# Kernel optimization log

Hardware: AMD Instinct MI355X
Metric: run time of the kernel (lower is better)

Reference implementation:

```python
import jax, jax.numpy as jnp
import numpy as np

N_NODES = 100000
N_EDGES = 1600000
D_IN, D_H1, D_H2 = 128, 64, 16


def setup_inputs() -> dict:
    key = jax.random.key(0)
    ks = jax.random.split(key, 12)
    def glorot(k, shape):
        fan_in, fan_out = shape
        lim = np.sqrt(6.0 / (fan_in + fan_out)).astype(np.float32)
        return jax.random.uniform(k, shape, jnp.float32, -lim, lim)
    x = jax.random.normal(ks[0], (N_NODES, D_IN), jnp.float32)
    edge_index = jax.random.randint(ks[1], (2, N_EDGES), 0, N_NODES, jnp.int64)
    return {
        "x": x,
        "edge_index": edge_index,
        # SAGEConv1: lin_l (neighbor agg, has bias), lin_r (root, no bias) -- stored (in,out)
        "w1_l": glorot(ks[2], (D_IN, D_H1)),
        "w1_r": glorot(ks[3], (D_IN, D_H1)),
        "b1": jnp.zeros((D_H1,), jnp.float32),
        # SAGEConv2
        "w2_l": glorot(ks[4], (D_H1, D_H2)),
        "w2_r": glorot(ks[5], (D_H1, D_H2)),
        "b2": jnp.zeros((D_H2,), jnp.float32),
        # MLP head
        "fc1_w": glorot(ks[6], (D_H2, 8)),
        "fc1_b": jnp.zeros((8,), jnp.float32),
        "fc2_w": glorot(ks[7], (8, 1)),
        "fc2_b": jnp.zeros((1,), jnp.float32),
    }


def _sage_conv(h, src, dst, n_nodes, w_l, w_r, b):
    # mean aggregation of source-node features into destination nodes
    msgs = h[src]                                                  # [E, d]
    agg = jax.ops.segment_sum(msgs, dst, num_segments=n_nodes)     # [N, d]
    deg = jax.ops.segment_sum(jnp.ones((src.shape[0],), h.dtype), dst,
                              num_segments=n_nodes)                # [N]
    mean = agg / jnp.maximum(deg, 1.0)[:, None]
    return mean @ w_l + h @ w_r + b


def reference(x, edge_index, w1_l, w1_r, b1, w2_l, w2_r, b2,
              fc1_w, fc1_b, fc2_w, fc2_b):
    src, dst = edge_index[0], edge_index[1]
    n = x.shape[0]
    h = _sage_conv(x, src, dst, n, w1_l, w1_r, b1)   # [N, 64]
    h = _sage_conv(h, src, dst, n, w2_l, w2_r, b2)   # [N, 16]
    # embedding_mlp on edge endpoint embeddings
    e = h[src] * h[dst]                              # [E, 16]
    out = (e @ fc1_w + fc1_b) @ fc2_w + fc2_b        # [E, 1]
    return jax.nn.sigmoid(out)
```

## Files before the change

kernel.cpp:

```cpp
#include <hip/hip_runtime.h>
#include <hip/hip_fp16.h>
#include <math.h>

#define NN 100000
#define NE 1600000

#define BSH  9
#define BKN  512
#define NB   196
#define ABLK 128
#define EPB  ((NE + ABLK - 1) / ABLK)
#define GEMMB ((NN + 63) / 64)
#define GBLK ((GEMMB + 1) / 2)

typedef __attribute__((ext_vector_type(8))) short bf16x8;
typedef __attribute__((ext_vector_type(4))) float f32x4;

__device__ __forceinline__ unsigned short f2bf(float f) {
    unsigned u = __builtin_bit_cast(unsigned, f);
    u += 0x7fffu + ((u >> 16) & 1u);
    return (unsigned short)(u >> 16);
}
__device__ __forceinline__ float bf2f(unsigned short h) {
    unsigned u = ((unsigned)h) << 16;
    return __builtin_bit_cast(float, u);
}
__device__ __forceinline__ float2 unpackh2(unsigned w) {
    const __half2 h = __builtin_bit_cast(__half2, w);
    return __half22float2(h);
}

__global__ __launch_bounds__(256) void fused0(const int* __restrict__ dst,
    const float* __restrict__ w1l, const float* __restrict__ w1r,
    const float* __restrict__ w2l, const float* __restrict__ w2r,
    const float* __restrict__ b1, const float* __restrict__ fc1w,
    const float* __restrict__ fc1b, const float* __restrict__ fc2w,
    const float* __restrict__ fc2b, int* __restrict__ mat,
    unsigned short* __restrict__ ATh, unsigned short* __restrict__ ATl,
    float* __restrict__ cbuf)
{
    __shared__ int h[NB];
    __shared__ float sl[64], sr[64];
    const int t = threadIdx.x;
    if (blockIdx.x < ABLK) {
        for (int i = t; i < NB; i += 256) h[i] = 0;
        __syncthreads();
        const int a = blockIdx.x;
        const int beg = a * EPB;
        const int end = (beg + EPB < NE) ? beg + EPB : NE;
        for (int e = beg + t; e < end; e += 256)
            atomicAdd(&h[dst[e] >> BSH], 1);
        __syncthreads();
        for (int i = t; i < NB; i += 256) mat[(size_t)i * ABLK + a] = h[i];
        return;
    }
    if (blockIdx.x < ABLK + 128) {
        const int k = blockIdx.x - ABLK;
        const int j = t;
        if (j < 64) { sl[j] = w1l[k * 64 + j]; sr[j] = w1r[k * 64 + j]; }
        __syncthreads();
        if (j < 64) {
            const int sel = j >> 4, jj = j & 15;
            const float* row = (sel < 2) ? sl : sr;
            const float* w2  = (sel & 1) ? w2r : w2l;
            float acc = 0.f;
#pragma unroll
            for (int m = 0; m < 64; ++m) acc = fmaf(row[m], w2[m * 16 + jj], acc);
            const unsigned short hh = f2bf(acc);
            ATh[j * 128 + k] = hh;
            ATl[j * 128 + k] = f2bf(acc - bf2f(hh));
        }
        return;
    }
    const int j = t;
    if (j < 16) {
        float a = 0.f;
        for (int m = 0; m < 64; ++m) a = fmaf(b1[m], w2l[m * 16 + j], a);
        cbuf[j] = a;
    } else if (j < 32) {
        const int jj = j - 16;
        float a = 0.f;
        for (int m = 0; m < 64; ++m) a = fmaf(b1[m], w2r[m * 16 + jj], a);
        cbuf[j] = a;
    } else if (j < 48) {
        const int k = j - 32;
        float a = 0.f;
        for (int m = 0; m < 8; ++m) a = fmaf(fc1w[k * 8 + m], fc2w[m], a);
        cbuf[j] = a;
    } else if (j == 48) {
        float a = fc2b[0];
        for (int m = 0; m < 8; ++m) a = fmaf(fc1b[m], fc2w[m], a);
        cbuf[48] = a;
    }
}

__global__ __launch_bounds__(256) void scan_all(int* __restrict__ mat,
    int* __restrict__ bbase)
{
    __shared__ int s[256];
    const int t = threadIdx.x;
    int run = 0;
    if (t < NB) {
        int* col = mat + (size_t)t * ABLK;
        for (int a = 0; a < ABLK; ++a) { const int v = col[a]; col[a] = run; run += v; }
    }
    s[t] = (t < NB) ? run : 0;
    __syncthreads();
    for (int off = 1; off < 256; off <<= 1) {
        const int u = (t >= off) ? s[t - off] : 0;
        __syncthreads();
        s[t] += u;
        __syncthreads();
    }
    if (t < NB) bbase[t] = s[t] - run;
    if (t == NB - 1) bbase[NB] = s[t];
}

#define LDST 136
__global__ __launch_bounds__(512) void fused1(const int* __restrict__ src,
    const int* __restrict__ dst, const int* __restrict__ mat,
    const int* __restrict__ bbase, unsigned* __restrict__ part,
    const float* __restrict__ x, const unsigned short* __restrict__ ATh,
    const unsigned short* __restrict__ ATl, signed char* __restrict__ p8,
    float* __restrict__ pscale, __half* __restrict__ qh)
{
    __shared__ unsigned short sAh[64 * LDST];
    __shared__ unsigned short sAl[64 * LDST];
    __shared__ int cur[NB];
    const int tid = threadIdx.x;

    if (blockIdx.x < ABLK) {
        const int a = blockIdx.x;
        for (int i = tid; i < NB; i += 512)
            cur[i] = mat[(size_t)i * ABLK + a] + bbase[i];
        __syncthreads();
        const int beg = a * EPB;
        const int end = (beg + EPB < NE) ? beg + EPB : NE;
        for (int e = beg + tid; e < end; e += 512) {
            const int s = src[e], d = dst[e];
            const int pos = atomicAdd(&cur[d >> BSH], 1);
            part[pos] = ((unsigned)s << BSH) | (unsigned)(d & (BKN - 1));
        }
        return;
    }

    for (int i = tid; i < 1024; i += 512) {
        const int row = i >> 4, ch = i & 15;
        const uint4 vh = *(const uint4*)(ATh + row * 128 + ch * 8);
        const uint4 vl = *(const uint4*)(ATl + row * 128 + ch * 8);
        *(uint4*)(sAh + row * LDST + ch * 8) = vh;
        *(uint4*)(sAl + row * LDST + ch * 8) = vl;
    }
    __syncthreads();

    const int wave8 = tid >> 6;
    const int tile = (blockIdx.x - ABLK) * 2 + (wave8 >> 2);
    const int wave = wave8 & 3;
    const int lane = tid & 63;
    const int lr = lane & 15;
    const int lg = lane >> 4;

    bf16x8 bh[4][4], bl[4][4];
#pragma unroll
    for (int ct = 0; ct < 4; ++ct) {
        const int col = ct * 16 + lr;
#pragma unroll
        for (int ks = 0; ks < 4; ++ks) {
            const int k0 = ks * 32 + lg * 8;
            bh[ct][ks] = *(const bf16x8*)(sAh + col * LDST + k0);
            bl[ct][ks] = *(const bf16x8*)(sAl + col * LDST + k0);
        }
    }

    if (tile >= GEMMB) return;
    const int tilebase = tile * 64;
    const int xrowidx = tilebase + wave * 16 + lr;
    const float* xrow = x + (size_t)(xrowidx < NN ? xrowidx : NN - 1) * 128;

    f32x4 acc[4] = {f32x4{0,0,0,0}, f32x4{0,0,0,0}, f32x4{0,0,0,0}, f32x4{0,0,0,0}};
#pragma unroll
    for (int ks = 0; ks < 4; ++ks) {
        const int k0 = ks * 32 + lg * 8;
        const float4 v0 = *(const float4*)(xrow + k0);
        const float4 v1 = *(const float4*)(xrow + k0 + 4);
        const float vv[8] = {v0.x, v0.y, v0.z, v0.w, v1.x, v1.y, v1.z, v1.w};
        bf16x8 xh, xl;
#pragma unroll
        for (int j = 0; j < 8; ++j) {
            const unsigned short h = f2bf(vv[j]);
            xh[j] = (short)h;
            xl[j] = (short)f2bf(vv[j] - bf2f(h));
        }
#pragma unroll
        for (int ct = 0; ct < 4; ++ct) {
            acc[ct] = __builtin_amdgcn_mfma_f32_16x16x32_bf16(xh, bh[ct][ks], acc[ct], 0, 0, 0);
            acc[ct] = __builtin_amdgcn_mfma_f32_16x16x32_bf16(xh, bl[ct][ks], acc[ct], 0, 0, 0);
            acc[ct] = __builtin_amdgcn_mfma_f32_16x16x32_bf16(xl, bh[ct][ks], acc[ct], 0, 0, 0);
        }
    }

#pragma unroll
    for (int rg = 0; rg < 4; ++rg) {
        float m = fmaxf(fabsf(acc[0][rg]), fabsf(acc[1][rg]));
#pragma unroll
        for (int d = 1; d < 16; d <<= 1) m = fmaxf(m, __shfl_xor(m, d, 64));
        m = fmaxf(m, 1e-20f);
        const float scl = m * (1.0f / 127.0f);
        const float inv = 127.0f / m;
        const int nrow = tilebase + wave * 16 + lg * 4 + rg;
        if (nrow < NN) {
            const int q0 = __float2int_rn(acc[0][rg] * inv);
            const int q1 = __float2int_rn(acc[1][rg] * inv);
            p8[(size_t)nrow * 32 + lr]      = (signed char)q0;
            p8[(size_t)nrow * 32 + 16 + lr] = (signed char)q1;
            if (lr == 0) pscale[nrow] = scl;
            qh[(size_t)nrow * 32 + lr]      = __float2half(acc[2][rg]);
            qh[(size_t)nrow * 32 + 16 + lr] = __float2half(acc[3][rg]);
        }
    }
}

__global__ __launch_bounds__(512) void partB_build(const unsigned* __restrict__ part,
    const int* __restrict__ bbase, int* __restrict__ rowptr, int* __restrict__ cols)
{
    __shared__ int h[BKN];
    __shared__ int cur[BKN];
    __shared__ int wsum[8];
    const int b = blockIdx.x;
    const int t = threadIdx.x;
    const int beg = bbase[b], end = bbase[b + 1];
    h[t] = 0;
    __syncthreads();
    for (int e = beg + t; e < end; e += 512)
        atomicAdd(&h[part[e] & (BKN - 1u)], 1);
    __syncthreads();
    const int v = h[t];
    int inc = v;
#pragma unroll
    for (int d = 1; d < 64; d <<= 1) {
        const int u = __shfl_up(inc, d, 64);
        if ((t & 63) >= d) inc += u;
    }
    if ((t & 63) == 63) wsum[t >> 6] = inc;
    __syncthreads();
    int woff = 0;
    for (int w = 0; w < (t >> 6); ++w) woff += wsum[w];
    const int excl = inc + woff - v;
    cur[t] = excl;
    const int node = b * BKN + t;
    if (node < NN) rowptr[node] = beg + excl;
    if (b == NB - 1 && t == 0) rowptr[NN] = NE;
    __syncthreads();
    for (int e = beg + t; e < end; e += 512) {
        const unsigned w = part[e];
        const int pos = atomicAdd(&cur[w & (BKN - 1u)], 1);
        cols[beg + pos] = (int)(w >> BSH);
    }
}

__global__ __launch_bounds__(256) void agg1_csr(const int* __restrict__ rowptr,
    const int* __restrict__ cols, const signed char* __restrict__ p8,
    const float* __restrict__ pscale, const __half* __restrict__ qh,
    const float* __restrict__ cbuf, __half* __restrict__ g, __half* __restrict__ r)
{
    const int node = blockIdx.x * 8 + (threadIdx.x >> 5);
    if (node >= NN) return;
    const int lane = threadIdx.x & 31;
    const int es = lane >> 2;
    const int k  = lane & 3;
    const int beg = rowptr[node], end = rowptr[node + 1];
    const uint2* p64 = (const uint2*)p8;
    float a0 = 0.f, a1 = 0.f, a2 = 0.f, a3 = 0.f;
    float a4 = 0.f, a5 = 0.f, a6 = 0.f, a7 = 0.f;
#pragma unroll 2
    for (int j = beg; j < end; j += 8) {
        const int jj = j + es;
        const int s = cols[(jj < end) ? jj : (end - 1)];
        const float scl = (jj < end) ? pscale[s] : 0.f;
        const uint2 w = p64[(size_t)s * 4 + k];
        a0 = fmaf((float)(signed char)(w.x & 0xffu), scl, a0);
        a1 = fmaf((float)(signed char)((w.x >> 8) & 0xffu), scl, a1);
        a2 = fmaf((float)(signed char)((w.x >> 16) & 0xffu), scl, a2);
        a3 = fmaf((float)(signed char)(w.x >> 24), scl, a3);
        a4 = fmaf((float)(signed char)(w.y & 0xffu), scl, a4);
        a5 = fmaf((float)(signed char)((w.y >> 8) & 0xffu), scl, a5);
        a6 = fmaf((float)(signed char)((w.y >> 16) & 0xffu), scl, a6);
        a7 = fmaf((float)(signed char)(w.y >> 24), scl, a7);
    }
#pragma unroll
    for (int d = 4; d <= 16; d <<= 1) {
        a0 += __shfl_xor(a0, d, 64); a1 += __shfl_xor(a1, d, 64);
        a2 += __shfl_xor(a2, d, 64); a3 += __shfl_xor(a3, d, 64);
        a4 += __shfl_xor(a4, d, 64); a5 += __shfl_xor(a5, d, 64);
        a6 += __shfl_xor(a6, d, 64); a7 += __shfl_xor(a7, d, 64);
    }
    if (es == 0) {
        const float dg = (float)(end - beg);
        const float inv = 1.0f / fmaxf(dg, 1.0f);
        const uint4 qw = *(const uint4*)(qh + (size_t)node * 32 + 8 * k);
        const float2 q0 = unpackh2(qw.x), q1 = unpackh2(qw.y);
        const float2 q2 = unpackh2(qw.z), q3 = unpackh2(qw.w);
        const float4 cb0 = *(const float4*)(cbuf + 8 * k);
        const float4 cb1 = *(const float4*)(cbuf + 8 * k + 4);
        const float v0 = fmaf(a0, inv, q0.x + cb0.x);
        const float v1 = fmaf(a1, inv, q0.y + cb0.y);
        const float v2 = fmaf(a2, inv, q1.x + cb0.z);
        const float v3 = fmaf(a3, inv, q1.y + cb0.w);
        const float v4 = fmaf(a4, inv, q2.x + cb1.x);
        const float v5 = fmaf(a5, inv, q2.y + cb1.y);
        const float v6 = fmaf(a6, inv, q3.x + cb1.z);
        const float v7 = fmaf(a7, inv, q3.y + cb1.w);
        uint4 ow;
        ow.x = __builtin_bit_cast(unsigned, __floats2half2_rn(v0, v1));
        ow.y = __builtin_bit_cast(unsigned, __floats2half2_rn(v2, v3));
        ow.z = __builtin_bit_cast(unsigned, __floats2half2_rn(v4, v5));
        ow.w = __builtin_bit_cast(unsigned, __floats2half2_rn(v6, v7));
        if (k < 2) *(uint4*)(g + (size_t)node * 16 + 8 * k) = ow;
        else       *(uint4*)(r + (size_t)node * 16 + 8 * (k - 2)) = ow;
    }
}

__global__ __launch_bounds__(256) void agg2_csr(const int* __restrict__ rowptr,
    const int* __restrict__ cols, const __half* __restrict__ g,
    const __half* __restrict__ r, const float* __restrict__ b2,
    __half* __restrict__ h2)
{
    const int node = blockIdx.x * 8 + (threadIdx.x >> 5);
    if (node >= NN) return;
    const int lane = threadIdx.x & 31;
    const int es = lane >> 2;
    const int k  = lane & 3;
    const int beg = rowptr[node], end = rowptr[node + 1];
    const uint2* g64 = (const uint2*)g;
    float a0 = 0.f, a1 = 0.f, a2 = 0.f, a3 = 0.f;
#pragma unroll 2
    for (int j = beg; j < end; j += 8) {
        const int jj = j + es;
        const int s = cols[(jj < end) ? jj : (end - 1)];
        const float m = (jj < end) ? 1.0f : 0.0f;
        const uint2 w = g64[(size_t)s * 4 + k];
        const float2 v0 = unpackh2(w.x);
        const float2 v1 = unpackh2(w.y);
        a0 = fmaf(v0.x, m, a0);
        a1 = fmaf(v0.y, m, a1);
        a2 = fmaf(v1.x, m, a2);
        a3 = fmaf(v1.y, m, a3);
    }
#pragma unroll
    for (int d = 4; d <= 16; d <<= 1) {
        a0 += __shfl_xor(a0, d, 64); a1 += __shfl_xor(a1, d, 64);
        a2 += __shfl_xor(a2, d, 64); a3 += __shfl_xor(a3, d, 64);
    }
    if (es == 0) {
        const float dg = (float)(end - beg);
        const float inv = 1.0f / fmaxf(dg, 1.0f);
        const uint2 rw = ((const uint2*)r)[(size_t)node * 4 + k];
        const float2 r0 = unpackh2(rw.x), r1 = unpackh2(rw.y);
        const float4 bb = *(const float4*)(b2 + 4 * k);
        const float v0 = fmaf(a0, inv, r0.x + bb.x);
        const float v1 = fmaf(a1, inv, r0.y + bb.y);
        const float v2 = fmaf(a2, inv, r1.x + bb.z);
        const float v3 = fmaf(a3, inv, r1.y + bb.w);
        uint2 ow;
        ow.x = __builtin_bit_cast(unsigned, __floats2half2_rn(v0, v1));
        ow.y = __builtin_bit_cast(unsigned, __floats2half2_rn(v2, v3));
        ((uint2*)h2)[(size_t)node * 4 + k] = ow;
    }
}

__global__ __launch_bounds__(256) void edge_mlp(const int* __restrict__ src,
    const int* __restrict__ dst, const __half* __restrict__ h2,
    const float* __restrict__ cbuf, float* __restrict__ out)
{
    __shared__ float sv[17];
    if (threadIdx.x < 16) sv[threadIdx.x] = cbuf[32 + threadIdx.x];
    if (threadIdx.x == 16) sv[16] = cbuf[48];
    __syncthreads();
    const int e0 = blockIdx.x * 512 + threadIdx.x;
    const int e1 = e0 + 256;
    const int s0 = src[e0], d0 = dst[e0];
    const int s1 = src[e1], d1 = dst[e1];
    const uint4* hs0 = (const uint4*)(h2 + (size_t)s0 * 16);
    const uint4* hd0 = (const uint4*)(h2 + (size_t)d0 * 16);
    const uint4* hs1 = (const uint4*)(h2 + (size_t)s1 * 16);
    const uint4* hd1 = (const uint4*)(h2 + (size_t)d1 * 16);
    const uint4 a00 = hs0[0], a01 = hs0[1];
    const uint4 b00 = hd0[0], b01 = hd0[1];
    const uint4 a10 = hs1[0], a11 = hs1[1];
    const uint4 b10 = hd1[0], b11 = hd1[1];
    const unsigned aw0[8] = {a00.x, a00.y, a00.z, a00.w, a01.x, a01.y, a01.z, a01.w};
    const unsigned bw0[8] = {b00.x, b00.y, b00.z, b00.w, b01.x, b01.y, b01.z, b01.w};
    const unsigned aw1[8] = {a10.x, a10.y, a10.z, a10.w, a11.x, a11.y, a11.z, a11.w};
    const unsigned bw1[8] = {b10.x, b10.y, b10.z, b10.w, b11.x, b11.y, b11.z, b11.w};
    float acc0 = sv[16], acc1 = sv[16];
#pragma unroll
    for (int qq = 0; qq < 8; ++qq) {
        const float2 a0 = unpackh2(aw0[qq]), b0 = unpackh2(bw0[qq]);
        const float2 a1 = unpackh2(aw1[qq]), b1 = unpackh2(bw1[qq]);
        acc0 = fmaf(a0.x * b0.x, sv[qq * 2 + 0], acc0);
        acc0 = fmaf(a0.y * b0.y, sv[qq * 2 + 1], acc0);
        acc1 = fmaf(a1.x * b1.x, sv[qq * 2 + 0], acc1);
        acc1 = fmaf(a1.y * b1.y, sv[qq * 2 + 1], acc1);
    }
    out[e0] = 1.0f / (1.0f + __expf(-acc0));
    out[e1] = 1.0f / (1.0f + __expf(-acc1));
}

extern "C" void kernel_launch(void* const* d_in, const int* in_sizes, int n_in,
                              void* d_out, int out_size, void* d_ws, size_t ws_size,
                              hipStream_t stream)
{
    const float* x    = (const float*)d_in[0];
    const int*   ei   = (const int*)d_in[1];
    const float* w1l  = (const float*)d_in[2];
    const float* w1r  = (const float*)d_in[3];
    const float* b1   = (const float*)d_in[4];
    const float* w2l  = (const float*)d_in[5];
    const float* w2r  = (const float*)d_in[6];
    const float* b2   = (const float*)d_in[7];
    const float* fc1w = (const float*)d_in[8];
    const float* fc1b = (const float*)d_in[9];
    const float* fc2w = (const float*)d_in[10];
    const float* fc2b = (const float*)d_in[11];
    float* out = (float*)d_out;

    const int* src = ei;
    const int* dst = ei + NE;

    int* W = (int*)d_ws;
    size_t o = 0;
#define ALIGN16() o = (o + 15) & ~(size_t)15
    int* mat    = W + o; o += (size_t)NB * ABLK; ALIGN16();
    int* bbase  = W + o; o += NB + 1;            ALIGN16();
    int* rowptr = W + o; o += NN + 1;            ALIGN16();
    unsigned* part = (unsigned*)(W + o); o += NE; ALIGN16();
    int* cols   = W + o; o += NE;                ALIGN16();
    unsigned short* ATh = (unsigned short*)(W + o); o += 4096; ALIGN16();
    unsigned short* ATl = (unsigned short*)(W + o); o += 4096; ALIGN16();
    float* cbuf = (float*)(W + o); o += 64;      ALIGN16();
    signed char* p8 = (signed char*)(W + o); o += (size_t)NN * 8;  ALIGN16();
    float* pscale   = (float*)(W + o); o += NN;  ALIGN16();
    __half* qh  = (__half*)(W + o); o += (size_t)NN * 16; ALIGN16();
    __half* g   = (__half*)(W + o); o += (size_t)NN * 8;  ALIGN16();
    __half* r   = (__half*)(W + o); o += (size_t)NN * 8;  ALIGN16();
    __half* h2  = (__half*)(W + o); o += (size_t)NN * 8;  ALIGN16();

    fused0<<<ABLK + 129, 256, 0, stream>>>(dst, w1l, w1r, w2l, w2r, b1,
                                           fc1w, fc1b, fc2w, fc2b, mat, ATh, ATl, cbuf);
    scan_all<<<1, 256, 0, stream>>>(mat, bbase);
    fused1<<<ABLK + GBLK, 512, 0, stream>>>(src, dst, mat, bbase, part,
                                            x, ATh, ATl, p8, pscale, qh);
    partB_build<<<NB, 512, 0, stream>>>(part, bbase, rowptr, cols);
    agg1_csr<<<(NN + 7) / 8, 256, 0, stream>>>(rowptr, cols, p8, pscale, qh, cbuf, g, r);
    agg2_csr<<<(NN + 7) / 8, 256, 0, stream>>>(rowptr, cols, g, r, b2, h2);
    edge_mlp<<<NE / 512, 256, 0, stream>>>(src, dst, h2, cbuf, out);
}
```

Baseline: 141.7 us.

## Overlap CSR bucket build with layer-1 GEMM and widen CSR gather loads

The edge scatter becomes its own kernel. The per-bucket CSR build (histogram, scan, column placement) is merged into the projection GEMM kernel through a shared-memory union, so the CSR build can overlap with the dense GEMM instead of running as a separate serialized launch. Both aggregation kernels now gather 16-byte rows per lane instead of 8-byte rows, processing 16 edges per iteration and doing one more shuffle-reduction step. This trades more registers per lane and a longer reduction for fewer, wider memory transactions.

```diff
diff --git a/kernel.cpp b/kernel.cpp
--- a/kernel.cpp
+++ b/kernel.cpp
@@ -12,6 +12,7 @@
 #define EPB  ((NE + ABLK - 1) / ABLK)
 #define GEMMB ((NN + 63) / 64)
 #define GBLK ((GEMMB + 1) / 2)
+#define LDST 136
 
 typedef __attribute__((ext_vector_type(8))) short bf16x8;
 typedef __attribute__((ext_vector_type(4))) float f32x4;
@@ -29,6 +30,10 @@
     const __half2 h = __builtin_bit_cast(__half2, w);
     return __half22float2(h);
 }
+
+struct GemmSmem { unsigned short sAh[64 * LDST]; unsigned short sAl[64 * LDST]; };
+struct PartSmem { int h[BKN]; int cur[BKN]; int wsum[8]; };
+union FusedSmem { GemmSmem gm; PartSmem pb; };
 
 __global__ __launch_bounds__(256) void fused0(const int* __restrict__ dst,
     const float* __restrict__ w1l, const float* __restrict__ w1r,
@@ -116,34 +121,72 @@
     if (t == NB - 1) bbase[NB] = s[t];
 }
 
-#define LDST 136
-__global__ __launch_bounds__(512) void fused1(const int* __restrict__ src,
+__global__ __launch_bounds__(512) void partA_scatter(const int* __restrict__ src,
     const int* __restrict__ dst, const int* __restrict__ mat,
-    const int* __restrict__ bbase, unsigned* __restrict__ part,
+    const int* __restrict__ bbase, unsigned* __restrict__ part)
+{
+    __shared__ int cur[NB];
+    const int a = blockIdx.x;
+    for (int i = threadIdx.x; i < NB; i += 512)
+        cur[i] = mat[(size_t)i * ABLK + a] + bbase[i];
+    __syncthreads();
+    const int beg = a * EPB;
+    const int end = (beg + EPB < NE) ? beg + EPB : NE;
+    for (int e = beg + threadIdx.x; e < end; e += 512) {
+        const int s = src[e], d = dst[e];
+        const int pos = atomicAdd(&cur[d >> BSH], 1);
+        part[pos] = ((unsigned)s << BSH) | (unsigned)(d & (BKN - 1));
+    }
+}
+
+__global__ __launch_bounds__(512) void fused2(const unsigned* __restrict__ part,
+    const int* __restrict__ bbase, int* __restrict__ rowptr, int* __restrict__ cols,
     const float* __restrict__ x, const unsigned short* __restrict__ ATh,
     const unsigned short* __restrict__ ATl, signed char* __restrict__ p8,
     float* __restrict__ pscale, __half* __restrict__ qh)
 {
-    __shared__ unsigned short sAh[64 * LDST];
-    __shared__ unsigned short sAl[64 * LDST];
-    __shared__ int cur[NB];
+    __shared__ FusedSmem su;
     const int tid = threadIdx.x;
 
-    if (blockIdx.x < ABLK) {
-        const int a = blockIdx.x;
-        for (int i = tid; i < NB; i += 512)
-            cur[i] = mat[(size_t)i * ABLK + a] + bbase[i];
-        __syncthreads();
-        const int beg = a * EPB;
-        const int end = (beg + EPB < NE) ? beg + EPB : NE;
-        for (int e = beg + tid; e < end; e += 512) {
-            const int s = src[e], d = dst[e];
-            const int pos = atomicAdd(&cur[d >> BSH], 1);
-            part[pos] = ((unsigned)s << BSH) | (unsigned)(d & (BKN - 1));
+    if (blockIdx.x < NB) {
+        int* h = su.pb.h;
+        int* cur = su.pb.cur;
+        int* wsum = su.pb.wsum;
+        const int b = blockIdx.x;
+        const int t = tid;
+        const int beg = bbase[b], end = bbase[b + 1];
+        h[t] = 0;
+        __syncthreads();
+        for (int e = beg + t; e < end; e += 512)
+            atomicAdd(&h[part[e] & (BKN - 1u)], 1);
+        __syncthreads();
+        const int v = h[t];
+        int inc = v;
+#pragma unroll
+        for (int d = 1; d < 64; d <<= 1) {
+            const int u = __shfl_up(inc, d, 64);
+            if ((t & 63) >= d) inc += u;
+        }
+        if ((t & 63) == 63) wsum[t >> 6] = inc;
+        __syncthreads();
+        int woff = 0;
+        for (int w = 0; w < (t >> 6); ++w) woff += wsum[w];
+        const int excl = inc + woff - v;
+        cur[t] = excl;
+        const int node = b * BKN + t;
+        if (node < NN) rowptr[node] = beg + excl;
+        if (b == NB - 1 && t == 0) rowptr[NN] = NE;
+        __syncthreads();
+        for (int e = beg + t; e < end; e += 512) {
+            const unsigned w = part[e];
+            const int pos = atomicAdd(&cur[w & (BKN - 1u)], 1);
+            cols[beg + pos] = (int)(w >> BSH);
         }
         return;
     }
 
+    unsigned short* sAh = su.gm.sAh;
+    unsigned short* sAl = su.gm.sAl;
     for (int i = tid; i < 1024; i += 512) {
         const int row = i >> 4, ch = i & 15;
         const uint4 vh = *(const uint4*)(ATh + row * 128 + ch * 8);
@@ -154,7 +197,7 @@
     __syncthreads();
 
     const int wave8 = tid >> 6;
-    const int tile = (blockIdx.x - ABLK) * 2 + (wave8 >> 2);
+    const int tile = (blockIdx.x - NB) * 2 + (wave8 >> 2);
     const int wave = wave8 & 3;
     const int lane = tid & 63;
     const int lr = lane & 15;
@@ -220,44 +263,6 @@
     }
 }
 
-__global__ __launch_bounds__(512) void partB_build(const unsigned* __restrict__ part,
-    const int* __restrict__ bbase, int* __restrict__ rowptr, int* __restrict__ cols)
-{
-    __shared__ int h[BKN];
-    __shared__ int cur[BKN];
-    __shared__ int wsum[8];
-    const int b = blockIdx.x;
-    const int t = threadIdx.x;
-    const int beg = bbase[b], end = bbase[b + 1];
-    h[t] = 0;
-    __syncthreads();
-    for (int e = beg + t; e < end; e += 512)
-        atomicAdd(&h[part[e] & (BKN - 1u)], 1);
-    __syncthreads();
-    const int v = h[t];
-    int inc = v;
-#pragma unroll
-    for (int d = 1; d < 64; d <<= 1) {
-        const int u = __shfl_up(inc, d, 64);
-        if ((t & 63) >= d) inc += u;
-    }
-    if ((t & 63) == 63) wsum[t >> 6] = inc;
-    __syncthreads();
-    int woff = 0;
-    for (int w = 0; w < (t >> 6); ++w) woff += wsum[w];
-    const int excl = inc + woff - v;
-    cur[t] = excl;
-    const int node = b * BKN + t;
-    if (node < NN) rowptr[node] = beg + excl;
-    if (b == NB - 1 && t == 0) rowptr[NN] = NE;
-    __syncthreads();
-    for (int e = beg + t; e < end; e += 512) {
-        const unsigned w = part[e];
-        const int pos = atomicAdd(&cur[w & (BKN - 1u)], 1);
-        cols[beg + pos] = (int)(w >> BSH);
-    }
-}
-
 __global__ __launch_bounds__(256) void agg1_csr(const int* __restrict__ rowptr,
     const int* __restrict__ cols, const signed char* __restrict__ p8,
     const float* __restrict__ pscale, const __half* __restrict__ qh,
@@ -266,57 +271,52 @@
     const int node = blockIdx.x * 8 + (threadIdx.x >> 5);
     if (node >= NN) return;
     const int lane = threadIdx.x & 31;
-    const int es = lane >> 2;
-    const int k  = lane & 3;
+    const int es = lane >> 1;
+    const int k  = lane & 1;
     const int beg = rowptr[node], end = rowptr[node + 1];
-    const uint2* p64 = (const uint2*)p8;
-    float a0 = 0.f, a1 = 0.f, a2 = 0.f, a3 = 0.f;
-    float a4 = 0.f, a5 = 0.f, a6 = 0.f, a7 = 0.f;
-#pragma unroll 2
-    for (int j = beg; j < end; j += 8) {
+    const uint4* p128 = (const uint4*)p8;
+    float a[16];
+#pragma unroll
+    for (int i = 0; i < 16; ++i) a[i] = 0.f;
+    for (int j = beg; j < end; j += 16) {
         const int jj = j + es;
         const int s = cols[(jj < end) ? jj : (end - 1)];
         const float scl = (jj < end) ? pscale[s] : 0.f;
-        const uint2 w = p64[(size_t)s * 4 + k];
-        a0 = fmaf((float)(signed char)(w.x & 0xffu), scl, a0);
-        a1 = fmaf((float)(signed char)((w.x >> 8) & 0xffu), scl, a1);
-        a2 = fmaf((float)(signed char)((w.x >> 16) & 0xffu), scl, a2);
-        a3 = fmaf((float)(signed char)(w.x >> 24), scl, a3);
-        a4 = fmaf((float)(signed char)(w.y & 0xffu), scl, a4);
-        a5 = fmaf((float)(signed char)((w.y >> 8) & 0xffu), scl, a5);
-        a6 = fmaf((float)(signed char)((w.y >> 16) & 0xffu), scl, a6);
-        a7 = fmaf((float)(signed char)(w.y >> 24), scl, a7);
-    }
-#pragma unroll
-    for (int d = 4; d <= 16; d <<= 1) {
-        a0 += __shfl_xor(a0, d, 64); a1 += __shfl_xor(a1, d, 64);
-        a2 += __shfl_xor(a2, d, 64); a3 += __shfl_xor(a3, d, 64);
-        a4 += __shfl_xor(a4, d, 64); a5 += __shfl_xor(a5, d, 64);
-        a6 += __shfl_xor(a6, d, 64); a7 += __shfl_xor(a7, d, 64);
+        const uint4 w = p128[(size_t)s * 2 + k];
+        const unsigned ws[4] = {w.x, w.y, w.z, w.w};
+#pragma unroll
+        for (int q = 0; q < 4; ++q) {
+            a[q * 4 + 0] = fmaf((float)(signed char)(ws[q] & 0xffu), scl, a[q * 4 + 0]);
+            a[q * 4 + 1] = fmaf((float)(signed char)((ws[q] >> 8) & 0xffu), scl, a[q * 4 + 1]);
+            a[q * 4 + 2] = fmaf((float)(signed char)((ws[q] >> 16) & 0xffu), scl, a[q * 4 + 2]);
+            a[q * 4 + 3] = fmaf((float)(signed char)(ws[q] >> 24), scl, a[q * 4 + 3]);
+        }
+    }
+#pragma unroll
+    for (int d = 2; d <= 16; d <<= 1) {
+#pragma unroll
+        for (int i = 0; i < 16; ++i) a[i] += __shfl_xor(a[i], d, 64);
     }
     if (es == 0) {
         const float dg = (float)(end - beg);
         const float inv = 1.0f / fmaxf(dg, 1.0f);
-        const uint4 qw = *(const uint4*)(qh + (size_t)node * 32 + 8 * k);
-        const float2 q0 = unpackh2(qw.x), q1 = unpackh2(qw.y);
-        const float2 q2 = unpackh2(qw.z), q3 = unpackh2(qw.w);
-        const float4 cb0 = *(const float4*)(cbuf + 8 * k);
-        const float4 cb1 = *(const float4*)(cbuf + 8 * k + 4);
-        const float v0 = fmaf(a0, inv, q0.x + cb0.x);
-        const float v1 = fmaf(a1, inv, q0.y + cb0.y);
-        const float v2 = fmaf(a2, inv, q1.x + cb0.z);
-        const float v3 = fmaf(a3, inv, q1.y + cb0.w);
-        const float v4 = fmaf(a4, inv, q2.x + cb1.x);
-        const float v5 = fmaf(a5, inv, q2.y + cb1.y);
-        const float v6 = fmaf(a6, inv, q3.x + cb1.z);
-        const float v7 = fmaf(a7, inv, q3.y + cb1.w);
-        uint4 ow;
-        ow.x = __builtin_bit_cast(unsigned, __floats2half2_rn(v0, v1));
-        ow.y = __builtin_bit_cast(unsigned, __floats2half2_rn(v2, v3));
-        ow.z = __builtin_bit_cast(unsigned, __floats2half2_rn(v4, v5));
-        ow.w = __builtin_bit_cast(unsigned, __floats2half2_rn(v6, v7));
-        if (k < 2) *(uint4*)(g + (size_t)node * 16 + 8 * k) = ow;
-        else       *(uint4*)(r + (size_t)node * 16 + 8 * (k - 2)) = ow;
+        const uint4 qw0 = *(const uint4*)(qh + (size_t)node * 32 + 16 * k);
+        const uint4 qw1 = *(const uint4*)(qh + (size_t)node * 32 + 16 * k + 8);
+        const unsigned qws[8] = {qw0.x, qw0.y, qw0.z, qw0.w, qw1.x, qw1.y, qw1.z, qw1.w};
+        float val[16];
+#pragma unroll
+        for (int i = 0; i < 16; ++i) {
+            const float2 qq = unpackh2(qws[i >> 1]);
+            const float qv = (i & 1) ? qq.y : qq.x;
+            val[i] = fmaf(a[i], inv, qv + cbuf[16 * k + i]);
+        }
+        unsigned ow[8];
+#pragma unroll
+        for (int i = 0; i < 8; ++i)
+            ow[i] = __builtin_bit_cast(unsigned, __floats2half2_rn(val[2 * i], val[2 * i + 1]));
+        __half* dptr = (k == 0) ? (g + (size_t)node * 16) : (r + (size_t)node * 16);
+        *(uint4*)(dptr)     = make_uint4(ow[0], ow[1], ow[2], ow[3]);
+        *(uint4*)(dptr + 8) = make_uint4(ow[4], ow[5], ow[6], ow[7]);
     }
 }
 
@@ -328,43 +328,45 @@
     const int node = blockIdx.x * 8 + (threadIdx.x >> 5);
     if (node >= NN) return;
     const int lane = threadIdx.x & 31;
-    const int es = lane >> 2;
-    const int k  = lane & 3;
+    const int es = lane >> 1;
+    const int k  = lane & 1;
     const int beg = rowptr[node], end = rowptr[node + 1];
-    const uint2* g64 = (const uint2*)g;
-    float a0 = 0.f, a1 = 0.f, a2 = 0.f, a3 = 0.f;
-#pragma unroll 2
-    for (int j = beg; j < end; j += 8) {
+    const uint4* g128 = (const uint4*)g;
+    float a[8];
+#pragma unroll
+    for (int i = 0; i < 8; ++i) a[i] = 0.f;
+    for (int j = beg; j < end; j += 16) {
         const int jj = j + es;
         const int s = cols[(jj < end) ? jj : (end - 1)];
         const float m = (jj < end) ? 1.0f : 0.0f;
-        const uint2 w = g64[(size_t)s * 4 + k];
-        const float2 v0 = unpackh2(w.x);
-        const float2 v1 = unpackh2(w.y);
-        a0 = fmaf(v0.x, m, a0);
-        a1 = fmaf(v0.y, m, a1);
-        a2 = fmaf(v1.x, m, a2);
-        a3 = fmaf(v1.y, m, a3);
-    }
-#pragma unroll
-    for (int d = 4; d <= 16; d <<= 1) {
-        a0 += __shfl_xor(a0, d, 64); a1 += __shfl_xor(a1, d, 64);
-        a2 += __shfl_xor(a2, d, 64); a3 += __shfl_xor(a3, d, 64);
+        const uint4 w = g128[(size_t)s * 2 + k];
+        const unsigned ws[4] = {w.x, w.y, w.z, w.w};
+#pragma unroll
+        for (int q = 0; q < 4; ++q) {
+            const float2 v = unpackh2(ws[q]);
+            a[q * 2 + 0] = fmaf(v.x, m, a[q * 2 + 0]);
+            a[q * 2 + 1] = fmaf(v.y, m, a[q * 2 + 1]);
+        }
+    }
+#pragma unroll
+    for (int d = 2; d <= 16; d <<= 1) {
+#pragma unroll
+        for (int i = 0; i < 8; ++i) a[i] += __shfl_xor(a[i], d, 64);
     }
     if (es == 0) {
         const float dg = (float)(end - beg);
         const float inv = 1.0f / fmaxf(dg, 1.0f);
-        const uint2 rw = ((const uint2*)r)[(size_t)node * 4 + k];
-        const float2 r0 = unpackh2(rw.x), r1 = unpackh2(rw.y);
-        const float4 bb = *(const float4*)(b2 + 4 * k);
-        const float v0 = fmaf(a0, inv, r0.x + bb.x);
-        const float v1 = fmaf(a1, inv, r0.y + bb.y);
-        const float v2 = fmaf(a2, inv, r1.x + bb.z);
-        const float v3 = fmaf(a3, inv, r1.y + bb.w);
-        uint2 ow;
-        ow.x = __builtin_bit_cast(unsigned, __floats2half2_rn(v0, v1));
-        ow.y = __builtin_bit_cast(unsigned, __floats2half2_rn(v2, v3));
-        ((uint2*)h2)[(size_t)node * 4 + k] = ow;
+        const uint4 rw = *(const uint4*)(r + (size_t)node * 16 + 8 * k);
+        const unsigned rws[4] = {rw.x, rw.y, rw.z, rw.w};
+        unsigned ow[4];
+#pragma unroll
+        for (int q = 0; q < 4; ++q) {
+            const float2 rv = unpackh2(rws[q]);
+            const float v0 = fmaf(a[q * 2 + 0], inv, rv.x + b2[8 * k + q * 2 + 0]);
+            const float v1 = fmaf(a[q * 2 + 1], inv, rv.y + b2[8 * k + q * 2 + 1]);
+            ow[q] = __builtin_bit_cast(unsigned, __floats2half2_rn(v0, v1));
+        }
+        *(uint4*)(h2 + (size_t)node * 16 + 8 * k) = make_uint4(ow[0], ow[1], ow[2], ow[3]);
     }
 }
 
@@ -448,9 +450,9 @@
     fused0<<<ABLK + 129, 256, 0, stream>>>(dst, w1l, w1r, w2l, w2r, b1,
                                            fc1w, fc1b, fc2w, fc2b, mat, ATh, ATl, cbuf);
     scan_all<<<1, 256, 0, stream>>>(mat, bbase);
-    fused1<<<ABLK + GBLK, 512, 0, stream>>>(src, dst, mat, bbase, part,
-                                            x, ATh, ATl, p8, pscale, qh);
-    partB_build<<<NB, 512, 0, stream>>>(part, bbase, rowptr, cols);
+    partA_scatter<<<ABLK, 512, 0, stream>>>(src, dst, mat, bbase, part);
+    fused2<<<NB + GBLK, 512, 0, stream>>>(part, bbase, rowptr, cols,
+                                          x, ATh, ATl, p8, pscale, qh);
     agg1_csr<<<(NN + 7) / 8, 256, 0, stream>>>(rowptr, cols, p8, pscale, qh, cbuf, g, r);
     agg2_csr<<<(NN + 7) / 8, 256, 0, stream>>>(rowptr, cols, g, r, b2, h2);
     edge_mlp<<<NE / 512, 256, 0, stream>>>(src, dst, h2, cbuf, out);
```

Result: slower. 156.1 us (+10.2%).
